# Performance work log

Hardware: AMD Instinct MI355X
Metric: run time of the kernel (lower is better)

Reference implementation:

```python
import jax, jax.numpy as jnp
import numpy as np

VOCAB, EMBED, HIDDEN, BATCH, SEQ = 32000, 512, 1024, 64, 512


def _xavier(key, shape):
    fan_out, fan_in = shape
    limit = float(np.sqrt(6.0 / (fan_in + fan_out)))
    return jax.random.uniform(key, shape, jnp.float32, -limit, limit)


def setup_inputs() -> dict:
    key = jax.random.key(0)
    ks = jax.random.split(key, 12)
    inp = {
        "texts": jax.random.randint(ks[0], (BATCH, SEQ), 0, VOCAB, dtype=jnp.int32),
        "emb": jax.random.normal(ks[1], (VOCAB, EMBED), jnp.float32),
        # layer 0: input_dim = EMBED
        "Wf0": _xavier(ks[2], (HIDDEN, EMBED + HIDDEN)), "bf0": jnp.zeros((HIDDEN,), jnp.float32),
        "Wi0": _xavier(ks[3], (HIDDEN, EMBED + HIDDEN)), "bi0": jnp.zeros((HIDDEN,), jnp.float32),
        "Wo0": _xavier(ks[4], (HIDDEN, EMBED + HIDDEN)), "bo0": jnp.zeros((HIDDEN,), jnp.float32),
        "Wc0": _xavier(ks[5], (HIDDEN, EMBED + HIDDEN)), "bc0": jnp.zeros((HIDDEN,), jnp.float32),
        # layer 1: input_dim = HIDDEN
        "Wf1": _xavier(ks[6], (HIDDEN, 2 * HIDDEN)), "bf1": jnp.zeros((HIDDEN,), jnp.float32),
        "Wi1": _xavier(ks[7], (HIDDEN, 2 * HIDDEN)), "bi1": jnp.zeros((HIDDEN,), jnp.float32),
        "Wo1": _xavier(ks[8], (HIDDEN, 2 * HIDDEN)), "bo1": jnp.zeros((HIDDEN,), jnp.float32),
        "Wc1": _xavier(ks[9], (HIDDEN, 2 * HIDDEN)), "bc1": jnp.zeros((HIDDEN,), jnp.float32),
        "Wy": _xavier(ks[10], (VOCAB, HIDDEN)), "by": jnp.zeros((VOCAB,), jnp.float32),
    }
    return inp


def _lstm_layer(xs, Wf, bf, Wi, bi, Wo, bo, Wc, bc):
    # xs: (T, B, F). torch.cat((h, x), dim=0) -> weight cols are [h | x].
    B = xs.shape[1]
    H = Wf.shape[0]
    h0 = jnp.zeros((B, H), xs.dtype)
    c0 = jnp.zeros((B, H), xs.dtype)

    def step(carry, x):
        h, c = carry
        concat = jnp.concatenate([h, x], axis=1)  # (B, H+F)
        ft = jax.nn.sigmoid(concat @ Wf.T + bf)
        it = jax.nn.sigmoid(concat @ Wi.T + bi)
        c_hat = jnp.tanh(concat @ Wc.T + bc)
        c = ft * c + it * c_hat
        ot = jax.nn.sigmoid(concat @ Wo.T + bo)
        h = ot * jnp.tanh(c)
        return (h, c), h

    (_, _), hs = jax.lax.scan(step, (h0, c0), xs)
    return hs  # (T, B, H)


def reference(texts, emb, Wf0, bf0, Wi0, bi0, Wo0, bo0, Wc0, bc0,
              Wf1, bf1, Wi1, bi1, Wo1, bo1, Wc1, bc1, Wy, by):
    # embedded: (T, B, E)
    xs = jnp.transpose(emb[texts], (1, 0, 2))
    hs0 = _lstm_layer(xs, Wf0, bf0, Wi0, bi0, Wo0, bo0, Wc0, bc0)
    hs1 = _lstm_layer(hs0, Wf1, bf1, Wi1, bi1, Wo1, bo1, Wc1, bc1)
    h_last = hs1[-1]  # (B, H) = last timestep of last layer (finetune=True branch)
    y = h_last @ Wy.T + by  # (B, VOCAB); .squeeze(1) in torch is a no-op for VOCAB>1
    return y
```

## Files before the change

### kernel.cpp

```cpp
#include <hip/hip_runtime.h>
#include <stdint.h>
#include <stddef.h>

#define T_SEQ  512
#define NBATCH 64
#define EMBED  512
#define HIDDEN 1024
#define VOCAB  32000
#define NWG    128
#define NTHR   256
#define AGENT  __HIP_MEMORY_SCOPE_AGENT
#define RING   260
#define SLOT_E (NBATCH * 2048)
#define BOUND  250

#define RST   66
#define PBUF  (64 * RST)

#define CNT(l, t) (cnt + ((((t) << 1) | (l)) << 5))

typedef __attribute__((ext_vector_type(8))) short short8;
typedef __attribute__((ext_vector_type(4))) float f32x4;

__device__ __forceinline__ unsigned short f2bf(float x) {
  union { float f; unsigned u; } v; v.f = x;
  unsigned r = v.u + 0x7FFFu + ((v.u >> 16) & 1u);
  return (unsigned short)(r >> 16);
}
__device__ __forceinline__ float sigm(float x) { return 1.0f / (1.0f + __expf(-x)); }
__device__ __forceinline__ float tanh_(float x) {
  float e = __expf(2.0f * x);
  return 1.0f - 2.0f / (e + 1.0f);
}

__device__ __forceinline__ void wait_ge(unsigned* p, unsigned tgt) {
  while (__hip_atomic_load(p, __ATOMIC_RELAXED, AGENT) < tgt)
    __builtin_amdgcn_s_sleep(1);
  __builtin_amdgcn_fence(__ATOMIC_ACQUIRE, "workgroup");
  asm volatile("" ::: "memory");
}

__global__ void embed_k(const int* __restrict__ texts, const float* __restrict__ emb,
                        unsigned short* __restrict__ xs) {
  const int bid = blockIdx.x;
  const int t = bid >> 6, b = bid & 63;
  const int row = texts[b * T_SEQ + t];
  const float* src = emb + (size_t)row * EMBED;
  const int e = threadIdx.x * 2;
  float2 v = *(const float2*)(src + e);
  unsigned pk = (unsigned)f2bf(v.x) | ((unsigned)f2bf(v.y) << 16);
  *(unsigned*)(xs + (size_t)bid * EMBED + e) = pk;
}

template<int LAYER>
__device__ __forceinline__ void run_layer(
    const unsigned short* __restrict__ xs_all,
    unsigned short* __restrict__ state,
    unsigned* __restrict__ cnt,
    const float* __restrict__ W0, const float* __restrict__ W1,
    const float* __restrict__ W2, const float* __restrict__ W3,
    const float* __restrict__ B0, const float* __restrict__ B1,
    const float* __restrict__ B2, const float* __restrict__ B3,
    float* buf, int w, int tid)
{
  constexpr int K  = LAYER ? 2048 : 1536;
  constexpr int KT = K / 128;
  const int lane = tid & 63;
  const int wid  = tid >> 6;
  const int ln   = lane & 15;
  const int qq   = lane >> 4;
  const int d0   = (tid & 7) * 2;
  const int bp   = (tid >> 3) * 2;
  const int gk0  = w * 16 + d0;

  short8 wreg[KT][4];
  const float* Wg[4] = {W0, W1, W2, W3};
  #pragma unroll
  for (int mt = 0; mt < 4; ++mt) {
    const float* row = Wg[mt] + (size_t)(w * 16 + ln) * K;
    #pragma unroll
    for (int kt = 0; kt < KT; ++kt) {
      int col;
      if (LAYER == 1) col = wid * 512 + kt * 32;
      else col = (kt < 4) ? (1024 + wid * 128 + kt * 32) : (wid * 256 + (kt - 4) * 32);
      col += qq * 8;
      f32x4 lo = *(const f32x4*)(row + col);
      f32x4 hi = *(const f32x4*)(row + col + 4);
      short8 v;
      v[0] = (short)f2bf(lo[0]); v[1] = (short)f2bf(lo[1]);
      v[2] = (short)f2bf(lo[2]); v[3] = (short)f2bf(lo[3]);
      v[4] = (short)f2bf(hi[0]); v[5] = (short)f2bf(hi[1]);
      v[6] = (short)f2bf(hi[2]); v[7] = (short)f2bf(hi[3]);
      wreg[kt][mt] = v;
    }
  }

  float bs[4][2];
  #pragma unroll
  for (int g = 0; g < 4; ++g) {
    const float* Bg = (g == 0) ? B0 : (g == 1) ? B1 : (g == 2) ? B2 : B3;
    bs[g][0] = Bg[gk0]; bs[g][1] = Bg[gk0 + 1];
  }
  float cst[2][2] = {{0.f, 0.f}, {0.f, 0.f}};

  wait_ge(CNT(0, 512), NWG);

  for (int t = 0; t < T_SEQ; ++t) {
    const int so  = t % RING;
    const int so1 = (t + 1) % RING;
    const unsigned short* slotT  = state + (size_t)so  * SLOT_E;
    const unsigned short* slotT1 = state + (size_t)so1 * SLOT_E;
    f32x4 acc[4][4] = {};

    if constexpr (LAYER == 0) {
      const unsigned short* xrow = xs_all + (size_t)t * (NBATCH * EMBED);
      #pragma unroll
      for (int kt = 0; kt < 4; ++kt) {
        const int bc = wid * 128 + kt * 32 + qq * 8;
        short8 bf[4];
        #pragma unroll
        for (int nt = 0; nt < 4; ++nt)
          bf[nt] = *(const short8*)(xrow + (size_t)(nt * 16 + ln) * EMBED + bc);
        #pragma unroll
        for (int mt = 0; mt < 4; ++mt)
          #pragma unroll
          for (int nt = 0; nt < 4; ++nt)
            acc[mt][nt] = __builtin_amdgcn_mfma_f32_16x16x32_bf16(
                wreg[kt][mt], bf[nt], acc[mt][nt], 0, 0, 0);
      }
      if (t > 0) wait_ge(CNT(0, t - 1), 64);
      const unsigned short* hbase = slotT + 1024;
      #pragma unroll
      for (int kt = 4; kt < KT; ++kt) {
        const int hc = wid * 256 + (kt - 4) * 32 + qq * 8;
        short8 bf[4];
        #pragma unroll
        for (int nt = 0; nt < 4; ++nt)
          bf[nt] = *(const short8*)(hbase + (size_t)(nt * 16 + ln) * 2048 + hc);
        #pragma unroll
        for (int mt = 0; mt < 4; ++mt)
          #pragma unroll
          for (int nt = 0; nt < 4; ++nt)
            acc[mt][nt] = __builtin_amdgcn_mfma_f32_16x16x32_bf16(
                wreg[kt][mt], bf[nt], acc[mt][nt], 0, 0, 0);
      }
    } else {
      if (wid >= 2)      wait_ge(CNT(0, t), 64);
      else if (t > 0)    wait_ge(CNT(1, t - 1), 64);
      const unsigned short* base = (wid < 2) ? slotT : slotT1;
      #pragma unroll
      for (int kt = 0; kt < KT; ++kt) {
        const int c = wid * 512 + kt * 32 + qq * 8;
        short8 bf[4];
        #pragma unroll
        for (int nt = 0; nt < 4; ++nt)
          bf[nt] = *(const short8*)(base + (size_t)(nt * 16 + ln) * 2048 + c);
        #pragma unroll
        for (int mt = 0; mt < 4; ++mt)
          #pragma unroll
          for (int nt = 0; nt < 4; ++nt)
            acc[mt][nt] = __builtin_amdgcn_mfma_f32_16x16x32_bf16(
                wreg[kt][mt], bf[nt], acc[mt][nt], 0, 0, 0);
      }
    }

    {
      float* bb = buf + wid * PBUF;
      #pragma unroll
      for (int mt = 0; mt < 4; ++mt)
        #pragma unroll
        for (int nt = 0; nt < 4; ++nt)
          #pragma unroll
          for (int j = 0; j < 4; ++j)
            bb[(mt * 16 + qq * 4 + j) * RST + nt * 16 + ln] = acc[mt][nt][j];
    }
    __syncthreads();

    float gv[4][2][2];
    #pragma unroll
    for (int gt = 0; gt < 4; ++gt)
      #pragma unroll
      for (int dd = 0; dd < 2; ++dd) {
        float sx = bs[gt][dd], sy = bs[gt][dd];
        #pragma unroll
        for (int p = 0; p < 4; ++p) {
          float2 v = *(const float2*)&buf[p * PBUF + (gt * 16 + d0 + dd) * RST + bp];
          sx += v.x; sy += v.y;
        }
        gv[gt][dd][0] = sx; gv[gt][dd][1] = sy;
      }

    if (LAYER == 0 && t >= BOUND)
      wait_ge(CNT(1, t - BOUND), 64);

    unsigned* su = (unsigned*)state;
    const size_t obase = (size_t)so1 * SLOT_E + (LAYER == 0 ? 1024 : 0) + gk0;
    #pragma unroll
    for (int s2 = 0; s2 < 2; ++s2) {
      cst[0][s2] = sigm(gv[0][0][s2]) * cst[0][s2] + sigm(gv[1][0][s2]) * tanh_(gv[3][0][s2]);
      cst[1][s2] = sigm(gv[0][1][s2]) * cst[1][s2] + sigm(gv[1][1][s2]) * tanh_(gv[3][1][s2]);
      const float h0v = sigm(gv[2][0][s2]) * tanh_(cst[0][s2]);
      const float h1v = sigm(gv[2][1][s2]) * tanh_(cst[1][s2]);
      const unsigned pk = (unsigned)f2bf(h0v) | ((unsigned)f2bf(h1v) << 16);
      __hip_atomic_store(su + ((obase + (size_t)(bp + s2) * 2048) >> 1), pk,
                         __ATOMIC_RELAXED, AGENT);
    }
    __syncthreads();
    if (tid == 0)
      __hip_atomic_fetch_add(CNT(LAYER, t), 1u, __ATOMIC_RELAXED, AGENT);
  }
}

__launch_bounds__(NTHR, 1)
__global__ void lstm_k(const unsigned short* __restrict__ xs,
                       unsigned short* __restrict__ state,
                       unsigned* __restrict__ cnt,
                       const float* __restrict__ Wf0, const float* __restrict__ Wi0,
                       const float* __restrict__ Wo0, const float* __restrict__ Wc0,
                       const float* __restrict__ bf0, const float* __restrict__ bi0,
                       const float* __restrict__ bo0, const float* __restrict__ bc0,
                       const float* __restrict__ Wf1, const float* __restrict__ Wi1,
                       const float* __restrict__ Wo1, const float* __restrict__ Wc1,
                       const float* __restrict__ bf1, const float* __restrict__ bi1,
                       const float* __restrict__ bo1, const float* __restrict__ bc1)
{
  __shared__ __align__(16) float buf[4 * PBUF];
  const int tid = threadIdx.x;
  const int gw  = blockIdx.x;

  {
    unsigned* su = (unsigned*)state;
    const int idx = gw * NTHR + tid;
    __hip_atomic_store(su + idx,         0u, __ATOMIC_RELAXED, AGENT);
    __hip_atomic_store(su + 32768 + idx, 0u, __ATOMIC_RELAXED, AGENT);
    __syncthreads();
    if (tid == 0)
      __hip_atomic_fetch_add(CNT(0, 512), 1u, __ATOMIC_RELAXED, AGENT);
  }

  if (gw < 64)
    run_layer<0>(xs, state, cnt, Wf0, Wi0, Wo0, Wc0, bf0, bi0, bo0, bc0,
                 buf, gw, tid);
  else
    run_layer<1>(nullptr, state, cnt, Wf1, Wi1, Wo1, Wc1, bf1, bi1, bo1, bc1,
                 buf, gw - 64, tid);
}

__global__ void final_k(const float* __restrict__ Wy,
                        const unsigned short* __restrict__ hlast,
                        const float* __restrict__ by,
                        float* __restrict__ out)
{
  const int tid = threadIdx.x, lane = tid & 63, wid = tid >> 6;
  const int ln = lane & 15, qq = lane >> 4;
  const int vbase = (blockIdx.x * 4 + wid) * 16;
  f32x4 acc[4] = {};
  const float* arow = Wy + (size_t)(vbase + ln) * HIDDEN;
  for (int kt = 0; kt < 32; ++kt) {
    const int kk = kt * 32 + qq * 8;
    f32x4 lo = *(const f32x4*)(arow + kk);
    f32x4 hi = *(const f32x4*)(arow + kk + 4);
    short8 a;
    a[0] = (short)f2bf(lo[0]); a[1] = (short)f2bf(lo[1]);
    a[2] = (short)f2bf(lo[2]); a[3] = (short)f2bf(lo[3]);
    a[4] = (short)f2bf(hi[0]); a[5] = (short)f2bf(hi[1]);
    a[6] = (short)f2bf(hi[2]); a[7] = (short)f2bf(hi[3]);
    #pragma unroll
    for (int nt = 0; nt < 4; ++nt) {
      short8 bv = *(const short8*)(hlast + (size_t)(nt * 16 + ln) * 2048 + kk);
      acc[nt] = __builtin_amdgcn_mfma_f32_16x16x32_bf16(a, bv, acc[nt], 0, 0, 0);
    }
  }
  const int v0 = vbase + qq * 4;
  const f32x4 bias = *(const f32x4*)(by + v0);
  #pragma unroll
  for (int nt = 0; nt < 4; ++nt) {
    const int bb = nt * 16 + ln;
    f32x4 r = acc[nt] + bias;
    *(f32x4*)(out + (size_t)bb * VOCAB + v0) = r;
  }
}

extern "C" void kernel_launch(void* const* d_in, const int* in_sizes, int n_in,
                              void* d_out, int out_size, void* d_ws, size_t ws_size,
                              hipStream_t stream) {
  (void)in_sizes; (void)n_in; (void)out_size; (void)ws_size;
  const int*   texts = (const int*)d_in[0];
  const float* emb   = (const float*)d_in[1];
  const float* Wf0 = (const float*)d_in[2];  const float* bf0 = (const float*)d_in[3];
  const float* Wi0 = (const float*)d_in[4];  const float* bi0 = (const float*)d_in[5];
  const float* Wo0 = (const float*)d_in[6];  const float* bo0 = (const float*)d_in[7];
  const float* Wc0 = (const float*)d_in[8];  const float* bc0 = (const float*)d_in[9];
  const float* Wf1 = (const float*)d_in[10]; const float* bf1 = (const float*)d_in[11];
  const float* Wi1 = (const float*)d_in[12]; const float* bi1 = (const float*)d_in[13];
  const float* Wo1 = (const float*)d_in[14]; const float* bo1 = (const float*)d_in[15];
  const float* Wc1 = (const float*)d_in[16]; const float* bc1 = (const float*)d_in[17];
  const float* Wy  = (const float*)d_in[18]; const float* by  = (const float*)d_in[19];

  char* ws = (char*)d_ws;
  unsigned*       cnt   = (unsigned*)ws;
  unsigned short* state = (unsigned short*)(ws + 262144);
  unsigned short* xs    = (unsigned short*)(ws + 262144 + (size_t)RING * SLOT_E * 2);
  float* out = (float*)d_out;

  hipMemsetAsync(cnt, 0, 135168, stream);
  embed_k<<<T_SEQ * NBATCH, 256, 0, stream>>>(texts, emb, xs);
  lstm_k<<<NWG, NTHR, 0, stream>>>(xs, state, cnt,
                                   Wf0, Wi0, Wo0, Wc0, bf0, bi0, bo0, bc0,
                                   Wf1, Wi1, Wo1, Wc1, bf1, bi1, bo1, bc1);
  final_k<<<VOCAB / 64, 256, 0, stream>>>(
      Wy, state + (size_t)(T_SEQ % RING) * SLOT_E, by, out);
}
```

Measured before the change: 5.326 ms.

## Split per-step LSTM barrier counters into chunked flags for finer-grained dataflow waits

Each timestep's single completion counter is replaced by 8 sub-flags, each covering a group of 8 workgroups. Consumers now wait only for the chunk of the hidden state they are about to multiply, and interleave those waits with MFMA work on chunks that are already ready. Flag values are loaded up front so waits on ready chunks are skipped. Layer 1 also bumps a separate aggregate counter that layer 0 uses for its ring-buffer write-after-read guard. The acquire fence after polling is dropped and the sleep interval raised, which saves a little per-poll cost but weakens the memory-ordering guarantee.

Result: slower. 5.776 ms (+8.5%).

```diff
diff --git a/kernel.cpp b/kernel.cpp
--- a/kernel.cpp
+++ b/kernel.cpp
@@ -17,7 +17,9 @@
 #define RST   66
 #define PBUF  (64 * RST)
 
-#define CNT(l, t) (cnt + ((((t) << 1) | (l)) << 5))
+#define FLG(cnt, l, t)  ((cnt) + ((((t) << 1) | (l)) << 5))
+#define AGG1(cnt, t)    ((cnt) + ((1024 + (t)) << 5))
+#define INITC(cnt)      ((cnt) + (1540 << 5))
 
 typedef __attribute__((ext_vector_type(8))) short short8;
 typedef __attribute__((ext_vector_type(4))) float f32x4;
@@ -33,11 +35,12 @@
   return 1.0f - 2.0f / (e + 1.0f);
 }
 
-__device__ __forceinline__ void wait_ge(unsigned* p, unsigned tgt) {
+__device__ __forceinline__ unsigned ld_flag(unsigned* p) {
+  return __hip_atomic_load(p, __ATOMIC_RELAXED, AGENT);
+}
+__device__ __forceinline__ void wait_flag(unsigned* p, unsigned tgt) {
   while (__hip_atomic_load(p, __ATOMIC_RELAXED, AGENT) < tgt)
-    __builtin_amdgcn_s_sleep(1);
-  __builtin_amdgcn_fence(__ATOMIC_ACQUIRE, "workgroup");
-  asm volatile("" ::: "memory");
+    __builtin_amdgcn_s_sleep(2);
 }
 
 __global__ void embed_k(const int* __restrict__ texts, const float* __restrict__ emb,
@@ -103,7 +106,8 @@
   }
   float cst[2][2] = {{0.f, 0.f}, {0.f, 0.f}};
 
-  wait_ge(CNT(0, 512), NWG);
+  wait_flag(INITC(cnt), NWG);
+  asm volatile("" ::: "memory");
 
   for (int t = 0; t < T_SEQ; ++t) {
     const int so  = t % RING;
@@ -112,7 +116,14 @@
     const unsigned short* slotT1 = state + (size_t)so1 * SLOT_E;
     f32x4 acc[4][4] = {};
 
+    unsigned war = 64;
+    if (LAYER == 0 && t >= BOUND) war = ld_flag(AGG1(cnt, t - BOUND));
+
     if constexpr (LAYER == 0) {
+      unsigned* flp = FLG(cnt, 0, (t > 0) ? t - 1 : 0) + 2 * wid;
+      unsigned fv[2] = {8u, 8u};
+      if (t > 0) { fv[0] = ld_flag(flp); fv[1] = ld_flag(flp + 1); }
+
       const unsigned short* xrow = xs_all + (size_t)t * (NBATCH * EMBED);
       #pragma unroll
       for (int kt = 0; kt < 4; ++kt) {
@@ -128,39 +139,56 @@
             acc[mt][nt] = __builtin_amdgcn_mfma_f32_16x16x32_bf16(
                 wreg[kt][mt], bf[nt], acc[mt][nt], 0, 0, 0);
       }
-      if (t > 0) wait_ge(CNT(0, t - 1), 64);
       const unsigned short* hbase = slotT + 1024;
       #pragma unroll
-      for (int kt = 4; kt < KT; ++kt) {
-        const int hc = wid * 256 + (kt - 4) * 32 + qq * 8;
-        short8 bf[4];
-        #pragma unroll
-        for (int nt = 0; nt < 4; ++nt)
-          bf[nt] = *(const short8*)(hbase + (size_t)(nt * 16 + ln) * 2048 + hc);
-        #pragma unroll
-        for (int mt = 0; mt < 4; ++mt)
+      for (int c = 0; c < 2; ++c) {
+        if (t > 0 && fv[c] < 8u) wait_flag(flp + c, 8u);
+        asm volatile("" ::: "memory");
+        #pragma unroll
+        for (int k2 = 0; k2 < 4; ++k2) {
+          const int kt = 4 + c * 4 + k2;
+          const int hc = wid * 256 + c * 128 + k2 * 32 + qq * 8;
+          short8 bf[4];
           #pragma unroll
           for (int nt = 0; nt < 4; ++nt)
-            acc[mt][nt] = __builtin_amdgcn_mfma_f32_16x16x32_bf16(
-                wreg[kt][mt], bf[nt], acc[mt][nt], 0, 0, 0);
+            bf[nt] = *(const short8*)(hbase + (size_t)(nt * 16 + ln) * 2048 + hc);
+          #pragma unroll
+          for (int mt = 0; mt < 4; ++mt)
+            #pragma unroll
+            for (int nt = 0; nt < 4; ++nt)
+              acc[mt][nt] = __builtin_amdgcn_mfma_f32_16x16x32_bf16(
+                  wreg[kt][mt], bf[nt], acc[mt][nt], 0, 0, 0);
+        }
       }
     } else {
-      if (wid >= 2)      wait_ge(CNT(0, t), 64);
-      else if (t > 0)    wait_ge(CNT(1, t - 1), 64);
+      unsigned* flp = (wid < 2) ? FLG(cnt, 1, (t > 0) ? t - 1 : 0) + 4 * wid
+                                : FLG(cnt, 0, t) + 4 * (wid - 2);
+      const bool need = (wid >= 2) || (t > 0);
+      unsigned fv[4] = {8u, 8u, 8u, 8u};
+      if (need) {
+        fv[0] = ld_flag(flp);     fv[1] = ld_flag(flp + 1);
+        fv[2] = ld_flag(flp + 2); fv[3] = ld_flag(flp + 3);
+      }
       const unsigned short* base = (wid < 2) ? slotT : slotT1;
       #pragma unroll
-      for (int kt = 0; kt < KT; ++kt) {
-        const int c = wid * 512 + kt * 32 + qq * 8;
-        short8 bf[4];
-        #pragma unroll
-        for (int nt = 0; nt < 4; ++nt)
-          bf[nt] = *(const short8*)(base + (size_t)(nt * 16 + ln) * 2048 + c);
-        #pragma unroll
-        for (int mt = 0; mt < 4; ++mt)
+      for (int c = 0; c < 4; ++c) {
+        if (need && fv[c] < 8u) wait_flag(flp + c, 8u);
+        asm volatile("" ::: "memory");
+        #pragma unroll
+        for (int k2 = 0; k2 < 4; ++k2) {
+          const int kt = c * 4 + k2;
+          const int cc = wid * 512 + c * 128 + k2 * 32 + qq * 8;
+          short8 bf[4];
           #pragma unroll
           for (int nt = 0; nt < 4; ++nt)
-            acc[mt][nt] = __builtin_amdgcn_mfma_f32_16x16x32_bf16(
-                wreg[kt][mt], bf[nt], acc[mt][nt], 0, 0, 0);
+            bf[nt] = *(const short8*)(base + (size_t)(nt * 16 + ln) * 2048 + cc);
+          #pragma unroll
+          for (int mt = 0; mt < 4; ++mt)
+            #pragma unroll
+            for (int nt = 0; nt < 4; ++nt)
+              acc[mt][nt] = __builtin_amdgcn_mfma_f32_16x16x32_bf16(
+                  wreg[kt][mt], bf[nt], acc[mt][nt], 0, 0, 0);
+        }
       }
     }
 
@@ -190,8 +218,8 @@
         gv[gt][dd][0] = sx; gv[gt][dd][1] = sy;
       }
 
-    if (LAYER == 0 && t >= BOUND)
-      wait_ge(CNT(1, t - BOUND), 64);
+    if (LAYER == 0 && t >= BOUND && war < 64)
+      wait_flag(AGG1(cnt, t - BOUND), 64);
 
     unsigned* su = (unsigned*)state;
     const size_t obase = (size_t)so1 * SLOT_E + (LAYER == 0 ? 1024 : 0) + gk0;
@@ -206,8 +234,12 @@
                          __ATOMIC_RELAXED, AGENT);
     }
     __syncthreads();
-    if (tid == 0)
-      __hip_atomic_fetch_add(CNT(LAYER, t), 1u, __ATOMIC_RELAXED, AGENT);
+    if (tid == 0) {
+      __hip_atomic_fetch_add(FLG(cnt, LAYER, t) + (w >> 3), 1u,
+                             __ATOMIC_RELAXED, AGENT);
+      if (LAYER == 1)
+        __hip_atomic_fetch_add(AGG1(cnt, t), 1u, __ATOMIC_RELAXED, AGENT);
+    }
   }
 }
 
@@ -235,7 +267,7 @@
     __hip_atomic_store(su + 32768 + idx, 0u, __ATOMIC_RELAXED, AGENT);
     __syncthreads();
     if (tid == 0)
-      __hip_atomic_fetch_add(CNT(0, 512), 1u, __ATOMIC_RELAXED, AGENT);
+      __hip_atomic_fetch_add(INITC(cnt), 1u, __ATOMIC_RELAXED, AGENT);
   }
 
   if (gw < 64)
@@ -303,7 +335,7 @@
   unsigned short* xs    = (unsigned short*)(ws + 262144 + (size_t)RING * SLOT_E * 2);
   float* out = (float*)d_out;
 
-  hipMemsetAsync(cnt, 0, 135168, stream);
+  hipMemsetAsync(cnt, 0, 262144, stream);
   embed_k<<<T_SEQ * NBATCH, 256, 0, stream>>>(texts, emb, xs);
   lstm_k<<<NWG, NTHR, 0, stream>>>(xs, state, cnt,
                                    Wf0, Wi0, Wo0, Wc0, bf0, bi0, bo0, bc0,
```

## Replace counter barriers with per-workgroup flag arrays and stream pre-cast bf16 weights

Applied to the files above, without the earlier changes.

Replaces the atomic fetch-add step counters with per-step flag arrays: each workgroup clears its own slot, and readers poll all 64 slots with a wave-wide any() check. A separate kernel casts all LSTM weights to bf16 in workspace. The recurrent kernel now keeps only 6 k-tiles of weights in registers and streams the rest from global memory each step, which lowers register pressure but adds per-step memory traffic. It also shrinks the state ring to 128 slots with a matching write-after-read guard, reads state with atomic 64-bit loads, and drains stores with an explicit vmcnt wait before signalling.

New measurement: 11.10 ms. +108.3%, slower.

```diff
diff --git a/kernel.cpp b/kernel.cpp
--- a/kernel.cpp
+++ b/kernel.cpp
@@ -10,14 +10,17 @@
 #define NWG    128
 #define NTHR   256
 #define AGENT  __HIP_MEMORY_SCOPE_AGENT
-#define RING   260
+#define RING   128
 #define SLOT_E (NBATCH * 2048)
-#define BOUND  250
+#define RB     120
+#define SENT   0xFFFFFFFFu
 
 #define RST   66
 #define PBUF  (64 * RST)
 
-#define CNT(l, t) (cnt + ((((t) << 1) | (l)) << 5))
+#define L0G   1572864
+#define L1G   2097152
+#define L1OFF 6291456
 
 typedef __attribute__((ext_vector_type(8))) short short8;
 typedef __attribute__((ext_vector_type(4))) float f32x4;
@@ -33,9 +36,20 @@
   return 1.0f - 2.0f / (e + 1.0f);
 }
 
-__device__ __forceinline__ void wait_ge(unsigned* p, unsigned tgt) {
-  while (__hip_atomic_load(p, __ATOMIC_RELAXED, AGENT) < tgt)
+__device__ __forceinline__ short8 ldb16(const unsigned short* p) {
+  union { unsigned long long q[2]; short8 v; } u;
+  u.q[0] = __hip_atomic_load((unsigned long long*)p,       __ATOMIC_RELAXED, AGENT);
+  u.q[1] = __hip_atomic_load((unsigned long long*)(p + 4), __ATOMIC_RELAXED, AGENT);
+  return u.v;
+}
+
+__device__ __forceinline__ void pollcan(unsigned* can, int idx, int lane) {
+  unsigned* cp = can + (idx << 6);
+  unsigned v = __hip_atomic_load(cp + lane, __ATOMIC_RELAXED, AGENT);
+  while (__any(v == SENT)) {
     __builtin_amdgcn_s_sleep(1);
+    v = __hip_atomic_load(cp + lane, __ATOMIC_RELAXED, AGENT);
+  }
   __builtin_amdgcn_fence(__ATOMIC_ACQUIRE, "workgroup");
   asm volatile("" ::: "memory");
 }
@@ -52,19 +66,48 @@
   *(unsigned*)(xs + (size_t)bid * EMBED + e) = pk;
 }
 
+__global__ void wcast_k(const float* __restrict__ f0, const float* __restrict__ f1,
+                        const float* __restrict__ f2, const float* __restrict__ f3,
+                        const float* __restrict__ f4, const float* __restrict__ f5,
+                        const float* __restrict__ f6, const float* __restrict__ f7,
+                        unsigned short* __restrict__ wb) {
+  const int b = blockIdx.x;
+  const float* src; size_t off, dst;
+  if (b < 3072) {
+    const int g = b / 768;
+    src = (g == 0) ? f0 : (g == 1) ? f1 : (g == 2) ? f2 : f3;
+    off = (size_t)(b % 768) * 2048;
+    dst = (size_t)g * L0G + off;
+  } else {
+    const int b2 = b - 3072, g = b2 / 1024;
+    src = (g == 0) ? f4 : (g == 1) ? f5 : (g == 2) ? f6 : f7;
+    off = (size_t)(b2 % 1024) * 2048;
+    dst = (size_t)L1OFF + (size_t)g * L1G + off;
+  }
+  const size_t i = off + (size_t)threadIdx.x * 8;
+  f32x4 lo = *(const f32x4*)(src + i);
+  f32x4 hi = *(const f32x4*)(src + i + 4);
+  short8 v;
+  v[0] = (short)f2bf(lo[0]); v[1] = (short)f2bf(lo[1]);
+  v[2] = (short)f2bf(lo[2]); v[3] = (short)f2bf(lo[3]);
+  v[4] = (short)f2bf(hi[0]); v[5] = (short)f2bf(hi[1]);
+  v[6] = (short)f2bf(hi[2]); v[7] = (short)f2bf(hi[3]);
+  *(short8*)(wb + dst + (size_t)threadIdx.x * 8) = v;
+}
+
 template<int LAYER>
 __device__ __forceinline__ void run_layer(
     const unsigned short* __restrict__ xs_all,
     unsigned short* __restrict__ state,
-    unsigned* __restrict__ cnt,
-    const float* __restrict__ W0, const float* __restrict__ W1,
-    const float* __restrict__ W2, const float* __restrict__ W3,
+    unsigned* __restrict__ can,
+    const unsigned short* __restrict__ wb,
     const float* __restrict__ B0, const float* __restrict__ B1,
     const float* __restrict__ B2, const float* __restrict__ B3,
     float* buf, int w, int tid)
 {
-  constexpr int K  = LAYER ? 2048 : 1536;
-  constexpr int KT = K / 128;
+  constexpr int K   = LAYER ? 2048 : 1536;
+  constexpr int KT  = K / 128;
+  constexpr int KTV = 6;
   const int lane = tid & 63;
   const int wid  = tid >> 6;
   const int ln   = lane & 15;
@@ -73,27 +116,26 @@
   const int bp   = (tid >> 3) * 2;
   const int gk0  = w * 16 + d0;
 
-  short8 wreg[KT][4];
-  const float* Wg[4] = {W0, W1, W2, W3};
+  const unsigned short* wrow[4];
   #pragma unroll
-  for (int mt = 0; mt < 4; ++mt) {
-    const float* row = Wg[mt] + (size_t)(w * 16 + ln) * K;
+  for (int mt = 0; mt < 4; ++mt)
+    wrow[mt] = wb + (LAYER ? (size_t)L1OFF + (size_t)mt * L1G
+                           : (size_t)mt * L0G)
+                  + (size_t)(w * 16 + ln) * K;
+
+  auto colw = [&](int kt) {
+    int c;
+    if (LAYER == 1) c = wid * 512 + kt * 32;
+    else c = (kt < 4) ? (1024 + wid * 128 + kt * 32) : (wid * 256 + (kt - 4) * 32);
+    return c + qq * 8;
+  };
+
+  short8 wreg[KTV][4];
+  #pragma unroll
+  for (int kt = 0; kt < KTV; ++kt)
     #pragma unroll
-    for (int kt = 0; kt < KT; ++kt) {
-      int col;
-      if (LAYER == 1) col = wid * 512 + kt * 32;
-      else col = (kt < 4) ? (1024 + wid * 128 + kt * 32) : (wid * 256 + (kt - 4) * 32);
-      col += qq * 8;
-      f32x4 lo = *(const f32x4*)(row + col);
-      f32x4 hi = *(const f32x4*)(row + col + 4);
-      short8 v;
-      v[0] = (short)f2bf(lo[0]); v[1] = (short)f2bf(lo[1]);
-      v[2] = (short)f2bf(lo[2]); v[3] = (short)f2bf(lo[3]);
-      v[4] = (short)f2bf(hi[0]); v[5] = (short)f2bf(hi[1]);
-      v[6] = (short)f2bf(hi[2]); v[7] = (short)f2bf(hi[3]);
-      wreg[kt][mt] = v;
-    }
-  }
+    for (int mt = 0; mt < 4; ++mt)
+      wreg[kt][mt] = *(const short8*)(wrow[mt] + colw(kt));
 
   float bs[4][2];
   #pragma unroll
@@ -103,15 +145,18 @@
   }
   float cst[2][2] = {{0.f, 0.f}, {0.f, 0.f}};
 
-  wait_ge(CNT(0, 512), NWG);
-
   for (int t = 0; t < T_SEQ; ++t) {
-    const int so  = t % RING;
-    const int so1 = (t + 1) % RING;
-    const unsigned short* slotT  = state + (size_t)so  * SLOT_E;
-    const unsigned short* slotT1 = state + (size_t)so1 * SLOT_E;
+    const unsigned short* slotT  = state + (size_t)(t % RING) * SLOT_E;
+    unsigned short*       slotT1 = state + (size_t)((t + 1) % RING) * SLOT_E;
+
+    bool war_ok = true;
+    if (LAYER == 0 && t >= RB) {
+      unsigned v = __hip_atomic_load(can + (((t - RB) * 2 + 1) << 6) + lane,
+                                     __ATOMIC_RELAXED, AGENT);
+      war_ok = !__any(v == SENT);
+    }
+
     f32x4 acc[4][4] = {};
-
     if constexpr (LAYER == 0) {
       const unsigned short* xrow = xs_all + (size_t)t * (NBATCH * EMBED);
       #pragma unroll
@@ -128,39 +173,50 @@
             acc[mt][nt] = __builtin_amdgcn_mfma_f32_16x16x32_bf16(
                 wreg[kt][mt], bf[nt], acc[mt][nt], 0, 0, 0);
       }
-      if (t > 0) wait_ge(CNT(0, t - 1), 64);
-      const unsigned short* hbase = slotT + 1024;
+      if (t > 0) pollcan(can, (t - 1) * 2 + 0, lane);
+      const unsigned short* hb = slotT + 1024;
       #pragma unroll
       for (int kt = 4; kt < KT; ++kt) {
+        const int col = colw(kt);
+        short8 wf[4];
+        #pragma unroll
+        for (int mt = 0; mt < 4; ++mt)
+          wf[mt] = (kt < KTV) ? wreg[kt < KTV ? kt : 0][mt]
+                              : *(const short8*)(wrow[mt] + col);
         const int hc = wid * 256 + (kt - 4) * 32 + qq * 8;
         short8 bf[4];
         #pragma unroll
         for (int nt = 0; nt < 4; ++nt)
-          bf[nt] = *(const short8*)(hbase + (size_t)(nt * 16 + ln) * 2048 + hc);
+          bf[nt] = ldb16(hb + (size_t)(nt * 16 + ln) * 2048 + hc);
         #pragma unroll
         for (int mt = 0; mt < 4; ++mt)
           #pragma unroll
           for (int nt = 0; nt < 4; ++nt)
             acc[mt][nt] = __builtin_amdgcn_mfma_f32_16x16x32_bf16(
-                wreg[kt][mt], bf[nt], acc[mt][nt], 0, 0, 0);
+                wf[mt], bf[nt], acc[mt][nt], 0, 0, 0);
       }
     } else {
-      if (wid >= 2)      wait_ge(CNT(0, t), 64);
-      else if (t > 0)    wait_ge(CNT(1, t - 1), 64);
+      if (wid < 2) { if (t > 0) pollcan(can, (t - 1) * 2 + 1, lane); }
+      else         { pollcan(can, t * 2 + 0, lane); }
       const unsigned short* base = (wid < 2) ? slotT : slotT1;
       #pragma unroll
       for (int kt = 0; kt < KT; ++kt) {
-        const int c = wid * 512 + kt * 32 + qq * 8;
+        const int col = colw(kt);
+        short8 wf[4];
+        #pragma unroll
+        for (int mt = 0; mt < 4; ++mt)
+          wf[mt] = (kt < KTV) ? wreg[kt < KTV ? kt : 0][mt]
+                              : *(const short8*)(wrow[mt] + col);
         short8 bf[4];
         #pragma unroll
         for (int nt = 0; nt < 4; ++nt)
-          bf[nt] = *(const short8*)(base + (size_t)(nt * 16 + ln) * 2048 + c);
+          bf[nt] = ldb16(base + (size_t)(nt * 16 + ln) * 2048 + col);
         #pragma unroll
         for (int mt = 0; mt < 4; ++mt)
           #pragma unroll
           for (int nt = 0; nt < 4; ++nt)
             acc[mt][nt] = __builtin_amdgcn_mfma_f32_16x16x32_bf16(
-                wreg[kt][mt], bf[nt], acc[mt][nt], 0, 0, 0);
+                wf[mt], bf[nt], acc[mt][nt], 0, 0, 0);
       }
     }
 
@@ -190,11 +246,12 @@
         gv[gt][dd][0] = sx; gv[gt][dd][1] = sy;
       }
 
-    if (LAYER == 0 && t >= BOUND)
-      wait_ge(CNT(1, t - BOUND), 64);
+    if (LAYER == 0 && t >= RB && !war_ok)
+      pollcan(can, (t - RB) * 2 + 1, lane);
 
     unsigned* su = (unsigned*)state;
-    const size_t obase = (size_t)so1 * SLOT_E + (LAYER == 0 ? 1024 : 0) + gk0;
+    const size_t obase = (size_t)((t + 1) % RING) * SLOT_E
+                       + (LAYER == 0 ? 1024 : 0) + gk0;
     #pragma unroll
     for (int s2 = 0; s2 < 2; ++s2) {
       cst[0][s2] = sigm(gv[0][0][s2]) * cst[0][s2] + sigm(gv[1][0][s2]) * tanh_(gv[3][0][s2]);
@@ -205,45 +262,31 @@
       __hip_atomic_store(su + ((obase + (size_t)(bp + s2) * 2048) >> 1), pk,
                          __ATOMIC_RELAXED, AGENT);
     }
+    asm volatile("s_waitcnt vmcnt(0)" ::: "memory");
     __syncthreads();
     if (tid == 0)
-      __hip_atomic_fetch_add(CNT(LAYER, t), 1u, __ATOMIC_RELAXED, AGENT);
+      __hip_atomic_store(can + ((t * 2 + LAYER) << 6) + w, 0u,
+                         __ATOMIC_RELAXED, AGENT);
   }
 }
 
 __launch_bounds__(NTHR, 1)
 __global__ void lstm_k(const unsigned short* __restrict__ xs,
                        unsigned short* __restrict__ state,
-                       unsigned* __restrict__ cnt,
-                       const float* __restrict__ Wf0, const float* __restrict__ Wi0,
-                       const float* __restrict__ Wo0, const float* __restrict__ Wc0,
+                       unsigned* __restrict__ can,
+                       const unsigned short* __restrict__ wb,
                        const float* __restrict__ bf0, const float* __restrict__ bi0,
                        const float* __restrict__ bo0, const float* __restrict__ bc0,
-                       const float* __restrict__ Wf1, const float* __restrict__ Wi1,
-                       const float* __restrict__ Wo1, const float* __restrict__ Wc1,
                        const float* __restrict__ bf1, const float* __restrict__ bi1,
                        const float* __restrict__ bo1, const float* __restrict__ bc1)
 {
   __shared__ __align__(16) float buf[4 * PBUF];
   const int tid = threadIdx.x;
   const int gw  = blockIdx.x;
-
-  {
-    unsigned* su = (unsigned*)state;
-    const int idx = gw * NTHR + tid;
-    __hip_atomic_store(su + idx,         0u, __ATOMIC_RELAXED, AGENT);
-    __hip_atomic_store(su + 32768 + idx, 0u, __ATOMIC_RELAXED, AGENT);
-    __syncthreads();
-    if (tid == 0)
-      __hip_atomic_fetch_add(CNT(0, 512), 1u, __ATOMIC_RELAXED, AGENT);
-  }
-
   if (gw < 64)
-    run_layer<0>(xs, state, cnt, Wf0, Wi0, Wo0, Wc0, bf0, bi0, bo0, bc0,
-                 buf, gw, tid);
+    run_layer<0>(xs, state, can, wb, bf0, bi0, bo0, bc0, buf, gw, tid);
   else
-    run_layer<1>(nullptr, state, cnt, Wf1, Wi1, Wo1, Wc1, bf1, bi1, bo1, bc1,
-                 buf, gw - 64, tid);
+    run_layer<1>(nullptr, state, can, wb, bf1, bi1, bo1, bc1, buf, gw - 64, tid);
 }
 
 __global__ void final_k(const float* __restrict__ Wy,
@@ -298,16 +341,17 @@
   const float* Wy  = (const float*)d_in[18]; const float* by  = (const float*)d_in[19];
 
   char* ws = (char*)d_ws;
-  unsigned*       cnt   = (unsigned*)ws;
+  unsigned*       can   = (unsigned*)ws;
   unsigned short* state = (unsigned short*)(ws + 262144);
-  unsigned short* xs    = (unsigned short*)(ws + 262144 + (size_t)RING * SLOT_E * 2);
+  unsigned short* xs    = (unsigned short*)(ws + 33816576);
+  unsigned short* wb    = (unsigned short*)(ws + 67371008);
   float* out = (float*)d_out;
 
-  hipMemsetAsync(cnt, 0, 135168, stream);
+  hipMemsetAsync(can, 0xFF, 262144, stream);
+  hipMemsetAsync(state, 0, SLOT_E * 2, stream);
   embed_k<<<T_SEQ * NBATCH, 256, 0, stream>>>(texts, emb, xs);
-  lstm_k<<<NWG, NTHR, 0, stream>>>(xs, state, cnt,
-                                   Wf0, Wi0, Wo0, Wc0, bf0, bi0, bo0, bc0,
-                                   Wf1, Wi1, Wo1, Wc1, bf1, bi1, bo1, bc1);
-  final_k<<<VOCAB / 64, 256, 0, stream>>>(
-      Wy, state + (size_t)(T_SEQ % RING) * SLOT_E, by, out);
-}
+  wcast_k<<<7168, 256, 0, stream>>>(Wf0, Wi0, Wo0, Wc0, Wf1, Wi1, Wo1, Wc1, wb);
+  lstm_k<<<NWG, NTHR, 0, stream>>>(xs, state, can, wb,
+                                   bf0, bi0, bo0, bc0, bf1, bi1, bo1, bc1);
+  final_k<<<VOCAB / 64, 256, 0, stream>>>(Wy, state, by, out);
+}
```
